# Kernel tuning notes

Hardware: AMD Instinct MI355X
Metric: run time of the kernel (lower is better)

Reference implementation:

```python
import jax, jax.numpy as jnp
import numpy as np
import math

NUM_ITER = 5
FEAT_STRIDE = 16
GAUSS_SIGMA = 1.0
HINGE_THRESHOLD = -999.0
MIN_FILTER_REG = 1e-3
ALPHA_EPS = 0.0


def apply_filter(feat, weights):
    # feat: (ni, ns, C, H, W); weights: (ns, C, fH, fW) -> scores (ni, ns, oH, oW)
    ni, ns, C, H, W = feat.shape
    fH, fW = weights.shape[-2], weights.shape[-1]
    x = feat.reshape(ni, ns * C, H, W)
    out = jax.lax.conv_general_dilated(
        x, weights, window_strides=(1, 1),
        padding=((fH // 2, fH // 2), (fW // 2, fW // 2)),
        dimension_numbers=('NCHW', 'OIHW', 'NCHW'),
        feature_group_count=ns)
    return out  # (ni, ns, oH, oW); oH = H + (fH+1)%2


def get_label(center, out_sz, sigma):
    # center: (ni, ns, 2) in (row, col) order
    k0 = jnp.arange(out_sz[0], dtype=jnp.float32)[None, None, :, None]
    k1 = jnp.arange(out_sz[1], dtype=jnp.float32)[None, None, None, :]
    g0 = jnp.exp(-0.5 / (sigma * sigma) * (k0 - center[..., 0][..., None, None]) ** 2)
    g1 = jnp.exp(-0.5 / (sigma * sigma) * (k1 - center[..., 1][..., None, None]) ** 2)
    return g0 * g1  # (ni, ns, oH, oW)


def _forward(weights, feat, bb, log_step_length, filter_reg):
    ni, ns = feat.shape[0], feat.shape[1]
    fH, fW = weights.shape[-2], weights.shape[-1]
    out_sz = (feat.shape[-2] + (fH + 1) % 2, feat.shape[-1] + (fW + 1) % 2)
    step = jnp.exp(log_step_length)[0]
    reg = jnp.maximum(filter_reg * filter_reg, MIN_FILTER_REG ** 2)[0]
    dmap_offset = jnp.array([fH % 2, fW % 2], jnp.float32) / 2.0
    # (x, y) -> (row, col), feature-grid coordinates
    center = ((bb[..., :2] + bb[..., 2:] / 2.0) / FEAT_STRIDE)[..., ::-1] - dmap_offset
    label = get_label(center, out_sz, GAUSS_SIGMA)
    mask = (label > HINGE_THRESHOLD).astype(feat.dtype)
    label = label * mask
    sw = math.sqrt(1.0 / ni)

    losses = []
    for _ in range(NUM_ITER):
        scores = apply_filter(feat, weights)
        scores_act = mask * scores + (1.0 - mask) * jax.nn.relu(scores)
        score_mask = mask + (1.0 - mask) * (jax.lax.stop_gradient(scores) > 0).astype(scores.dtype)
        residuals = sw * (scores_act - label)
        losses.append((jnp.sum(residuals ** 2) + reg * jnp.sum(weights ** 2)) / ns)
        residuals_mapped = score_mask * (sw * residuals)
        # feat-transpose = adjoint of apply_filter w.r.t. the filter weights
        _, vjp_fn = jax.vjp(lambda w: apply_filter(feat, w), weights)
        data_grad = vjp_fn(residuals_mapped)[0]
        weights_grad = data_grad + reg * weights
        scores_grad = apply_filter(feat, weights_grad)
        scores_grad = sw * (score_mask * scores_grad)
        alpha_num = jnp.sum(weights_grad ** 2, axis=(1, 2, 3))  # (ns,)
        alpha_den = jnp.maximum(
            jnp.sum(scores_grad.reshape(ni, ns, -1) ** 2, axis=(0, 2))
            + (reg + ALPHA_EPS) * alpha_num, 1e-8)
        alpha = alpha_num / alpha_den
        weights = weights - step * alpha[:, None, None, None] * weights_grad

    scores = apply_filter(feat, weights)
    scores = mask * scores + (1.0 - mask) * jax.nn.relu(scores)
    losses.append((jnp.sum((sw * (scores - label)) ** 2) + reg * jnp.sum(weights ** 2)) / ns)
    return weights, jnp.stack(losses)


def setup_inputs() -> dict:
    key = jax.random.key(0)
    k1, k2, k3, k4 = jax.random.split(key, 4)
    ni, ns, C, H, W, fH, fW = 3, 32, 512, 22, 22, 4, 4
    weights = 0.01 * jax.random.normal(k1, (ns, C, fH, fW), jnp.float32)
    feat = jax.random.normal(k2, (ni, ns, C, H, W), jnp.float32)
    # boxes (x, y, w, h) in image coords (image size = 22*16 = 352)
    xy = jax.random.uniform(k3, (ni, ns, 2), jnp.float32, 50.0, 250.0)
    wh = jax.random.uniform(k4, (ni, ns, 2), jnp.float32, 32.0, 96.0)
    bb = jnp.concatenate([xy, wh], axis=-1)
    log_step_length = jnp.zeros((1,), jnp.float32)  # log(1.0)
    filter_reg = 0.01 * jnp.ones((1,), jnp.float32)
    return {"weights": weights, "feat": feat, "bb": bb,
            "log_step_length": log_step_length, "filter_reg": filter_reg}


def reference(weights, feat, bb, log_step_length, filter_reg):
    return _forward(weights, feat, bb, log_step_length, filter_reg)
```

## Files before the change

### kernel.cpp

```cpp
#include <hip/hip_runtime.h>
#include <hip/hip_fp16.h>

#define NI 3
#define NS 32
#define CHN 512
#define OH 23
#define P2 529
#define NP 50784
#define UV 484
#define WSZ 262144
#define KTOT 1536
#define NKB 48
#define RSP 1544

typedef unsigned int uint32;
typedef unsigned short u16;
typedef _Float16 h2 __attribute__((ext_vector_type(2)));
typedef _Float16 f16x8 __attribute__((ext_vector_type(8)));
typedef float f32x4 __attribute__((ext_vector_type(4)));

#define OFF_FEATT 0UL
#define OFF_LABEL 47579136UL
#define OFF_S0    47782272UL
#define OFF_S1    47985408UL
#define OFF_SGRAW 48188544UL
#define OFF_WG    48391680UL
#define OFF_WGF16 49440256UL
#define OFF_W0F16 49964544UL
#define OFF_PART  50488832UL
#define OFF_FEATC 50521600UL
#define OFF_S0B   100853248UL
#define OFF_SGB   101056384UL

#define P_DEN   0
#define P_NUM   4320
#define P_LOSS  5600
#define P_WSQ0  5760
#define P_WSQA  5792
#define P_WSQ5  6816
#define P_L5    7840

__device__ __forceinline__ float waveSum(float v) {
#pragma unroll
  for (int o = 32; o > 0; o >>= 1) v += __shfl_xor(v, o, 64);
  return v;
}

__global__ __launch_bounds__(256) void k_setup(const float* __restrict__ feat,
                                               const float* __restrict__ w0,
                                               const float* __restrict__ bb,
                                               u16* __restrict__ featT,
                                               u16* __restrict__ w0f16,
                                               float* __restrict__ wmaster,
                                               float* __restrict__ label,
                                               float* __restrict__ part) {
  __shared__ uint32 lds32[64 * 121];
  __shared__ float sred[4];
  int b = blockIdx.x, tid = threadIdx.x;
  if (b < 1536) {
    int snT = b >> 4, r4 = b & 15;
    int cb = r4 >> 1, uvh = r4 & 1;
    int s = snT / 3, n = snT % 3;
    const float* fsrc =
        feat + ((size_t)n * NS + s) * CHN * UV + (size_t)(cb * 64) * UV + uvh * 242;
#pragma unroll
    for (int it = 0; it < 31; ++it) {
      int idx = it * 256 + tid;
      if (idx < 7744) {
        int r = (unsigned)idx / 121u;
        int j = idx - r * 121;
        float2 v = *(const float2*)(fsrc + (size_t)r * UV + 2 * j);
        lds32[idx] = (uint32)__half_as_ushort(__float2half(v.x)) |
                     ((uint32)__half_as_ushort(__float2half(v.y)) << 16);
      }
    }
    __syncthreads();
    uint32* dstT = (uint32*)featT +
                   ((size_t)(snT * 4 + (cb >> 1)) * UV + uvh * 242) * 64 + (cb & 1) * 32;
#pragma unroll
    for (int it = 0; it < 16; ++it) {
      int o = it * 256 + tid;
      if (o < 3872) {
        int uv = o >> 4, kp = o & 15;
        int j = uv >> 1, sh = (uv & 1) * 16;
        uint32 a0 = lds32[(4 * kp + 0) * 121 + j];
        uint32 a1 = lds32[(4 * kp + 1) * 121 + j];
        uint32 a2 = lds32[(4 * kp + 2) * 121 + j];
        uint32 a3 = lds32[(4 * kp + 3) * 121 + j];
        uint2 val;
        val.x = ((a0 >> sh) & 0xffffu) | (((a1 >> sh) & 0xffffu) << 16);
        val.y = ((a2 >> sh) & 0xffffu) | (((a3 >> sh) & 0xffffu) << 16);
        *(uint2*)(dstT + (size_t)uv * 64 + 2 * kp) = val;
      }
    }
  } else if (b < 1568) {
    int s = b - 1536;
    for (int i = tid; i < 8192; i += 256) {
      int tap = i >> 9, c = i & 511;
      w0f16[(size_t)s * 8192 + i] =
          __half_as_ushort(__float2half(w0[(size_t)s * 8192 + c * 16 + tap]));
    }
    float sq = 0.f;
    for (int i = tid; i < 8192; i += 256) {
      float v = w0[(size_t)s * 8192 + i];
      wmaster[(size_t)s * 8192 + i] = v;
      sq += v * v;
    }
    sq = waveSum(sq);
    if ((tid & 63) == 0) sred[tid >> 6] = sq;
    __syncthreads();
    if (tid == 0) part[P_WSQ0 + s] = sred[0] + sred[1] + sred[2] + sred[3];
  } else {
    int p = (b - 1568) * 256 + tid;
    if (p < NP) {
      int nsid = p / P2, rem = p % P2;
      int i = rem / OH, j = rem % OH;
      const float* bp = bb + (size_t)nsid * 4;
      float cr = (bp[1] + 0.5f * bp[3]) * 0.0625f;
      float cc = (bp[0] + 0.5f * bp[2]) * 0.0625f;
      float dy = (float)i - cr, dx = (float)j - cc;
      label[p] = __expf(-0.5f * (dy * dy + dx * dx));
    }
  }
}

__global__ __launch_bounds__(1024) void k_conv_fwd(const u16* __restrict__ featT,
                                                   const u16* __restrict__ wf16,
                                                   float* __restrict__ outA,
                                                   float* __restrict__ outB) {
  __shared__ uint32 w_lds[16 * 132];
  __shared__ float G[496 * 17];
  int tid = threadIdx.x;
  int bidx = blockIdx.x;
  int snT = bidx >> 1, ch = bidx & 1;
  int s = snT / 3, n = snT - s * 3;
  const uint32* wsrc = (const uint32*)(wf16 + (size_t)s * 8192) + ch * 128;
  for (int i = tid; i < 2048; i += 1024) {
    int tap = i >> 7, p = i & 127;
    w_lds[tap * 132 + p] = wsrc[(size_t)tap * 256 + p];
  }
  __syncthreads();
  int wave = tid >> 6, lane = tid & 63;
  int q = lane >> 4, m16 = lane & 15;
  int t0 = wave, t1 = wave + 16;
  bool has2 = (t1 < 31);
  f32x4 acc0 = {0.f, 0.f, 0.f, 0.f}, acc1 = {0.f, 0.f, 0.f, 0.f};
  size_t base = (size_t)snT * 4 * UV * 128;
  int r0i = t0 * 16 + m16;
  int r1i = has2 ? t1 * 16 + m16 : 483;
  if (r1i > 483) r1i = 483;
  size_t row0 = (size_t)r0i * 128;
  size_t row1 = (size_t)r1i * 128;
#pragma unroll
  for (int ks = 0; ks < 8; ++ks) {
    int cb = ch * 2 + (ks >> 2), cin = (ks & 3) * 32;
    size_t cbase = base + (size_t)cb * UV * 128 + cin + q * 8;
    f16x8 a0 = *(const f16x8*)(featT + cbase + row0);
    uint4 bw = *(const uint4*)&w_lds[m16 * 132 + ks * 16 + q * 4];
    f16x8 bf = __builtin_bit_cast(f16x8, bw);
    acc0 = __builtin_amdgcn_mfma_f32_16x16x32_f16(a0, bf, acc0, 0, 0, 0);
    if (has2) {
      f16x8 a1 = *(const f16x8*)(featT + cbase + row1);
      acc1 = __builtin_amdgcn_mfma_f32_16x16x32_f16(a1, bf, acc1, 0, 0, 0);
    }
  }
#pragma unroll
  for (int r = 0; r < 4; ++r) G[(t0 * 16 + q * 4 + r) * 17 + m16] = acc0[r];
  if (has2) {
#pragma unroll
    for (int r = 0; r < 4; ++r) G[(t1 * 16 + q * 4 + r) * 17 + m16] = acc1[r];
  }
  __syncthreads();
  if (tid < P2) {
    int y = tid / 23, x = tid - y * 23;
    float val = 0.f;
#pragma unroll
    for (int ky = 0; ky < 4; ++ky) {
      int u = y + ky - 2;
      if ((unsigned)u < 22u) {
#pragma unroll
        for (int kx = 0; kx < 4; ++kx) {
          int v = x + kx - 2;
          if ((unsigned)v < 22u) val += G[(u * 22 + v) * 17 + ky * 4 + kx];
        }
      }
    }
    float* dst = ch ? outB : outA;
    dst[(size_t)(n * NS + s) * P2 + tid] = val;
  }
}

__global__ __launch_bounds__(1024) void k_adjoint(
    int t, const float* __restrict__ feat, u16* __restrict__ featC,
    const float* __restrict__ label, const float* __restrict__ s0a,
    const float* __restrict__ s0b, const float* __restrict__ scores_old,
    float* __restrict__ scores_new, const float* __restrict__ sga,
    const float* __restrict__ sgb, float* __restrict__ wg, u16* __restrict__ wgf16,
    float* __restrict__ wmaster, float* __restrict__ part, const float* __restrict__ lsl,
    const float* __restrict__ fr) {
  __shared__ float r_lds[3 * P2];
  __shared__ __align__(16) u16 rs[16 * RSP];
  __shared__ __align__(16) float kred[3 * 4 * 64 * 4];
  __shared__ float lred[16], nred[16], wred[16], dend[16];
  int tid = threadIdx.x;
  int s = blockIdx.x >> 3, chunk = blockIdx.x & 7;
  int c0 = chunk * 64;
  float step = __expf(lsl[0]);
  float frv = fr[0];
  float reg = fmaxf(frv * frv, 1e-6f);

  float alpha_p = 0.f;
  if (t >= 1) {
    const float* np_ = part + P_NUM + (size_t)((t - 1) * NS + s) * 8;
    float nu = 0.f;
#pragma unroll
    for (int i = 0; i < 8; ++i) nu += np_[i];
    float dp = 0.f;
    for (int pl = tid; pl < 1587; pl += 1024) {
      int nn = (unsigned)pl / (unsigned)P2;
      int rem = pl - nn * P2;
      size_t gp = (size_t)(nn * NS + s) * P2 + rem;
      float g = sga[gp] + sgb[gp];
      dp += g * g;
    }
    dp = waveSum(dp);
    if ((tid & 63) == 0) dend[tid >> 6] = dp;
    __syncthreads();
    float de = 0.f;
#pragma unroll
    for (int i = 0; i < 16; ++i) de += dend[i];
    alpha_p = nu / fmaxf(de * (1.0f / 3.0f) + reg * nu, 1e-8f);
  }

  float lsum = 0.f;
  for (int pl = tid; pl < 1587; pl += 1024) {
    int nn = (unsigned)pl / (unsigned)P2;
    int rem = pl - nn * P2;
    size_t gp = (size_t)(nn * NS + s) * P2 + rem;
    float S = (t <= 1) ? (s0a[gp] + s0b[gp]) : scores_old[gp];
    if (t >= 1) S -= step * alpha_p * (sga[gp] + sgb[gp]);
    float d = S - label[gp];
    r_lds[nn * P2 + rem] = d * (1.0f / 3.0f);
    if (chunk == 0) {
      if (t >= 1) scores_new[gp] = S;
      lsum += d * d;
    }
  }
  lsum = waveSum(lsum);
  if ((tid & 63) == 0) lred[tid >> 6] = lsum;
  __syncthreads();
  if (chunk == 0 && tid == 0) {
    float L = 0.f;
#pragma unroll
    for (int i = 0; i < 16; ++i) L += lred[i];
    part[P_LOSS + t * NS + s] = L * (1.0f / 3.0f);
  }

  for (int idx = tid; idx < 16 * RSP; idx += 1024) {
    int tap = (unsigned)idx / (unsigned)RSP;
    int k = idx - tap * RSP;
    float val = 0.f;
    if (k < KTOT) {
      int n = k >> 9, uv = k & 511;
      if (uv < UV) {
        int u = (unsigned)uv / 22u;
        int v = uv - u * 22;
        int ky = tap >> 2, kx = tap & 3;
        int y = u + 2 - ky, x = v + 2 - kx;
        if ((unsigned)y < 23u && (unsigned)x < 23u) val = r_lds[n * P2 + y * OH + x];
      }
    }
    rs[idx] = __half_as_ushort(__float2half(val));
  }
  __syncthreads();

  int wave = tid >> 6, lane = tid & 63;
  int q = lane >> 4, m16 = lane & 15;
  int tile = wave & 3, kq = wave >> 2;
  int c = c0 + tile * 16 + m16;
  const u16* brow = rs + m16 * RSP + kq * 384 + q * 8;
  f32x4 acc = {0.f, 0.f, 0.f, 0.f};
  if (t == 0) {
#pragma unroll
    for (int ks = 0; ks < 12; ++ks) {
      int kb = kq * 12 + ks;
      int k0 = kb * 32 + q * 8;
      int nn = k0 >> 9, uv0 = k0 & 511;
      float v[8];
#pragma unroll
      for (int i = 0; i < 8; ++i) v[i] = 0.f;
      if (uv0 < UV) {
        const float* fsrc = feat + ((size_t)(nn * NS + s) * CHN + c) * UV + uv0;
        if (uv0 + 8 <= UV) {
          float4 p0 = *(const float4*)fsrc;
          float4 p1 = *(const float4*)(fsrc + 4);
          v[0] = p0.x; v[1] = p0.y; v[2] = p0.z; v[3] = p0.w;
          v[4] = p1.x; v[5] = p1.y; v[6] = p1.z; v[7] = p1.w;
        } else {
#pragma unroll
          for (int i = 0; i < 4; ++i) v[i] = fsrc[i];
        }
      }
      union { u16 h[8]; f16x8 f; uint4 u; } av;
#pragma unroll
      for (int i = 0; i < 8; ++i) av.h[i] = __half_as_ushort(__float2half(v[i]));
      *(uint4*)(featC + (((size_t)(s * NKB + kb) * CHN + c) * 32 + q * 8)) = av.u;
      f16x8 bf = *(const f16x8*)(brow + ks * 32);
      acc = __builtin_amdgcn_mfma_f32_16x16x32_f16(av.f, bf, acc, 0, 0, 0);
    }
  } else {
    const u16* arow = featC + ((size_t)(s * NKB + kq * 12) * CHN + c) * 32 + q * 8;
#pragma unroll
    for (int ks = 0; ks < 12; ++ks) {
      f16x8 a = *(const f16x8*)(arow + (size_t)ks * (CHN * 32));
      f16x8 bf = *(const f16x8*)(brow + ks * 32);
      acc = __builtin_amdgcn_mfma_f32_16x16x32_f16(a, bf, acc, 0, 0, 0);
    }
  }
  if (kq) *(f32x4*)&kred[(((kq - 1) * 4 + tile) * 64 + lane) * 4] = acc;
  __syncthreads();

  float num_part = 0.f, wsq_part = 0.f;
  if (kq == 0) {
#pragma unroll
    for (int kk = 0; kk < 3; ++kk)
      acc += *(const f32x4*)&kred[((kk * 4 + tile) * 64 + lane) * 4];
    int tap = m16;
    int ccb = c0 + tile * 16 + q * 4;
    union { u16 h[4]; uint2 v2; } pk;
#pragma unroll
    for (int r = 0; r < 4; ++r) {
      int cc = ccb + r;
      size_t widx = (size_t)s * 8192 + (size_t)cc * 16 + tap;
      float wold = wmaster[widx];
      float wnew = wold;
      if (t >= 1) {
        wnew = wold - step * alpha_p * wg[widx];
        wmaster[widx] = wnew;
      }
      float wgn = acc[r] + reg * wnew;
      wg[widx] = wgn;
      pk.h[r] = __half_as_ushort(__float2half(wgn));
      wsq_part += wnew * wnew;
      num_part += wgn * wgn;
    }
    *(uint2*)&wgf16[(size_t)s * 8192 + (size_t)tap * 512 + ccb] = pk.v2;
  }
  num_part = waveSum(num_part);
  wsq_part = waveSum(wsq_part);
  if (lane == 0) {
    nred[wave] = num_part;
    wred[wave] = wsq_part;
  }
  __syncthreads();
  if (tid == 0) {
    float nsum = 0.f, wsum = 0.f;
#pragma unroll
    for (int i = 0; i < 16; ++i) {
      nsum += nred[i];
      wsum += wred[i];
    }
    part[P_NUM + (size_t)(t * NS + s) * 8 + chunk] = nsum;
    if (t >= 1) part[P_WSQA + (size_t)((t - 1) * NS + s) * 8 + chunk] = wsum;
  }
}

__global__ __launch_bounds__(1024) void k_den(const float* __restrict__ sga,
                                              const float* __restrict__ sgb,
                                              float* __restrict__ part) {
  __shared__ float dend[16];
  int s = blockIdx.x, tid = threadIdx.x;
  float dp = 0.f;
  for (int pl = tid; pl < 1587; pl += 1024) {
    int nn = (unsigned)pl / (unsigned)P2;
    int rem = pl - nn * P2;
    size_t gp = (size_t)(nn * NS + s) * P2 + rem;
    float g = sga[gp] + sgb[gp];
    dp += g * g;
  }
  dp = waveSum(dp);
  if ((tid & 63) == 0) dend[tid >> 6] = dp;
  __syncthreads();
  if (tid == 0) {
    float de = 0.f;
#pragma unroll
    for (int i = 0; i < 16; ++i) de += dend[i];
    part[P_DEN + s] = de * (1.0f / 3.0f);
  }
}

__device__ __forceinline__ float alphaFinal(const float* __restrict__ part, int s,
                                            float reg) {
  const float* np_ = part + P_NUM + (size_t)(4 * NS + s) * 8;
  float nu = 0.f;
#pragma unroll
  for (int i = 0; i < 8; ++i) nu += np_[i];
  float de = part[P_DEN + s];
  return nu / fmaxf(de + reg * nu, 1e-8f);
}

__global__ void k_final(float* __restrict__ wmaster, const float* __restrict__ wg,
                        const float* __restrict__ scores4, const float* __restrict__ sga,
                        const float* __restrict__ sgb, const float* __restrict__ label,
                        float* __restrict__ part, const float* __restrict__ lsl,
                        const float* __restrict__ fr) {
  __shared__ float alpha_s[32];
  __shared__ float red4[4];
  int b = blockIdx.x, tid = threadIdx.x;
  float step = __expf(lsl[0]);
  float frv = fr[0];
  float reg = fmaxf(frv * frv, 1e-6f);
  if (tid < 32) alpha_s[tid] = alphaFinal(part, tid, reg);
  __syncthreads();
  if (b < 1024) {
    int idx = b * 256 + tid;
    int s = idx >> 13;
    float w5 = wmaster[idx] - step * alpha_s[s] * wg[idx];
    wmaster[idx] = w5;
    float sq = waveSum(w5 * w5);
    if ((tid & 63) == 0) red4[tid >> 6] = sq;
    __syncthreads();
    if (tid == 0) part[P_WSQ5 + b] = red4[0] + red4[1] + red4[2] + red4[3];
  } else {
    int p = (b - 1024) * 256 + tid;
    float contrib = 0.f;
    if (p < NP) {
      int nsid = p / P2;
      int s = nsid & 31;
      float s5 = scores4[p] - step * alpha_s[s] * (sga[p] + sgb[p]);
      float d = s5 - label[p];
      contrib = d * d;
    }
    contrib = waveSum(contrib);
    if ((tid & 63) == 0) red4[tid >> 6] = contrib;
    __syncthreads();
    if (tid == 0)
      part[P_L5 + (b - 1024)] = (red4[0] + red4[1] + red4[2] + red4[3]) * (1.0f / 3.0f);
  }
}

__global__ void k_losses(float* __restrict__ out_losses, const float* __restrict__ part,
                         const float* __restrict__ fr) {
  __shared__ float red[8];
  int tid = threadIdx.x;
  float frv = fr[0];
  float reg = fmaxf(frv * frv, 1e-6f);
  float v5 = 0.f;
  for (int i = tid; i < 1024; i += 256) v5 += part[P_WSQ5 + i];
  v5 = waveSum(v5);
  if ((tid & 63) == 0) red[tid >> 6] = v5;
  __syncthreads();
  float wsq5 = red[0] + red[1] + red[2] + red[3];
  float l5 = 0.f;
  for (int i = tid; i < 199; i += 256) l5 += part[P_L5 + i];
  l5 = waveSum(l5);
  if ((tid & 63) == 0) red[4 + (tid >> 6)] = l5;
  __syncthreads();
  float loss5 = red[4] + red[5] + red[6] + red[7];
  if (tid < 5) {
    int t = tid;
    float ls = 0.f;
    for (int i = 0; i < 32; ++i) ls += part[P_LOSS + t * NS + i];
    float ws_ = 0.f;
    if (t == 0) {
      for (int i = 0; i < 32; ++i) ws_ += part[P_WSQ0 + i];
    } else {
      for (int i = 0; i < 256; ++i) ws_ += part[P_WSQA + (t - 1) * 256 + i];
    }
    out_losses[t] = (ls + reg * ws_) * (1.0f / 32.0f);
  }
  if (tid == 5) out_losses[5] = (loss5 + reg * wsq5) * (1.0f / 32.0f);
}

extern "C" void kernel_launch(void* const* d_in, const int* in_sizes, int n_in,
                              void* d_out, int out_size, void* d_ws, size_t ws_size,
                              hipStream_t stream) {
  const float* w0 = (const float*)d_in[0];
  const float* feat = (const float*)d_in[1];
  const float* bb = (const float*)d_in[2];
  const float* lsl = (const float*)d_in[3];
  const float* fr = (const float*)d_in[4];
  float* out = (float*)d_out;
  char* ws = (char*)d_ws;
  u16* featT = (u16*)(ws + OFF_FEATT);
  float* label = (float*)(ws + OFF_LABEL);
  float* s0 = (float*)(ws + OFF_S0);
  float* s0b = (float*)(ws + OFF_S0B);
  float* s1 = (float*)(ws + OFF_S1);
  float* sga = (float*)(ws + OFF_SGRAW);
  float* sgb = (float*)(ws + OFF_SGB);
  float* wg = (float*)(ws + OFF_WG);
  u16* wgf16 = (u16*)(ws + OFF_WGF16);
  u16* w0f16 = (u16*)(ws + OFF_W0F16);
  float* part = (float*)(ws + OFF_PART);
  u16* featC = (u16*)(ws + OFF_FEATC);

  k_setup<<<1767, 256, 0, stream>>>(feat, w0, bb, featT, w0f16, out, label, part);
  k_conv_fwd<<<192, 1024, 0, stream>>>(featT, w0f16, s0, s0b);
  for (int t = 0; t < 5; ++t) {
    const float* so = (t <= 1) ? s0 : ((t & 1) ? s0 : s1);
    float* sn = (t & 1) ? s1 : s0;
    k_adjoint<<<256, 1024, 0, stream>>>(t, feat, featC, label, s0, s0b, so, sn, sga, sgb,
                                        wg, wgf16, out, part, lsl, fr);
    k_conv_fwd<<<192, 1024, 0, stream>>>(featT, wgf16, sga, sgb);
  }
  k_den<<<32, 1024, 0, stream>>>(sga, sgb, part);
  k_final<<<1223, 256, 0, stream>>>(out, wg, s0, sga, sgb, label, part, lsl, fr);
  k_losses<<<1, 256, 0, stream>>>(out + WSZ, part, fr);
}
```

Before: 356.1 us.

## Fuse k_den and k_losses into k_final with per-block alpha and ticket reduction

Removes the separate k_den and k_losses launches. Each k_final block now recomputes its spectrum's step-length denominator locally, and the last block to finish, found with an atomic ticket counter, does the final loss reduction. k_adjoint also caches the summed gradient scores in LDS so they are not reloaded from global memory. In exchange, 1223 blocks now each re-read 1587 gradient values, the atomic ticket adds a completion step, and k_adjoint uses more LDS.

```diff
diff --git a/kernel.cpp b/kernel.cpp
--- a/kernel.cpp
+++ b/kernel.cpp
@@ -32,13 +32,13 @@
 #define OFF_S0B   100853248UL
 #define OFF_SGB   101056384UL
 
-#define P_DEN   0
 #define P_NUM   4320
 #define P_LOSS  5600
 #define P_WSQ0  5760
 #define P_WSQA  5792
 #define P_WSQ5  6816
 #define P_L5    7840
+#define P_TICKET 8064
 
 __device__ __forceinline__ float waveSum(float v) {
 #pragma unroll
@@ -95,6 +95,7 @@
     }
   } else if (b < 1568) {
     int s = b - 1536;
+    if (b == 1536 && tid == 0) ((uint32*)part)[P_TICKET] = 0;
     for (int i = tid; i < 8192; i += 256) {
       int tap = i >> 9, c = i & 511;
       w0f16[(size_t)s * 8192 + i] =
@@ -199,6 +200,7 @@
     float* __restrict__ wmaster, float* __restrict__ part, const float* __restrict__ lsl,
     const float* __restrict__ fr) {
   __shared__ float r_lds[3 * P2];
+  __shared__ float g_lds[1587];
   __shared__ __align__(16) u16 rs[16 * RSP];
   __shared__ __align__(16) float kred[3 * 4 * 64 * 4];
   __shared__ float lred[16], nred[16], wred[16], dend[16];
@@ -221,6 +223,7 @@
       int rem = pl - nn * P2;
       size_t gp = (size_t)(nn * NS + s) * P2 + rem;
       float g = sga[gp] + sgb[gp];
+      g_lds[pl] = g;
       dp += g * g;
     }
     dp = waveSum(dp);
@@ -238,7 +241,7 @@
     int rem = pl - nn * P2;
     size_t gp = (size_t)(nn * NS + s) * P2 + rem;
     float S = (t <= 1) ? (s0a[gp] + s0b[gp]) : scores_old[gp];
-    if (t >= 1) S -= step * alpha_p * (sga[gp] + sgb[gp]);
+    if (t >= 1) S -= step * alpha_p * g_lds[pl];
     float d = S - label[gp];
     r_lds[nn * P2 + rem] = d * (1.0f / 3.0f);
     if (chunk == 0) {
@@ -365,13 +368,12 @@
   }
 }
 
-__global__ __launch_bounds__(1024) void k_den(const float* __restrict__ sga,
-                                              const float* __restrict__ sgb,
-                                              float* __restrict__ part) {
-  __shared__ float dend[16];
-  int s = blockIdx.x, tid = threadIdx.x;
+__device__ __forceinline__ float blockAlpha(int s, const float* __restrict__ sga,
+                                            const float* __restrict__ sgb,
+                                            const float* __restrict__ part, float reg,
+                                            int tid, float* ared) {
   float dp = 0.f;
-  for (int pl = tid; pl < 1587; pl += 1024) {
+  for (int pl = tid; pl < 1587; pl += 256) {
     int nn = (unsigned)pl / (unsigned)P2;
     int rem = pl - nn * P2;
     size_t gp = (size_t)(nn * NS + s) * P2 + rem;
@@ -379,97 +381,98 @@
     dp += g * g;
   }
   dp = waveSum(dp);
-  if ((tid & 63) == 0) dend[tid >> 6] = dp;
-  __syncthreads();
-  if (tid == 0) {
-    float de = 0.f;
-#pragma unroll
-    for (int i = 0; i < 16; ++i) de += dend[i];
-    part[P_DEN + s] = de * (1.0f / 3.0f);
-  }
-}
-
-__device__ __forceinline__ float alphaFinal(const float* __restrict__ part, int s,
-                                            float reg) {
+  __syncthreads();
+  if ((tid & 63) == 0) ared[tid >> 6] = dp;
+  __syncthreads();
+  float de = (ared[0] + ared[1] + ared[2] + ared[3]) * (1.0f / 3.0f);
   const float* np_ = part + P_NUM + (size_t)(4 * NS + s) * 8;
   float nu = 0.f;
 #pragma unroll
   for (int i = 0; i < 8; ++i) nu += np_[i];
-  float de = part[P_DEN + s];
   return nu / fmaxf(de + reg * nu, 1e-8f);
 }
 
-__global__ void k_final(float* __restrict__ wmaster, const float* __restrict__ wg,
-                        const float* __restrict__ scores4, const float* __restrict__ sga,
-                        const float* __restrict__ sgb, const float* __restrict__ label,
-                        float* __restrict__ part, const float* __restrict__ lsl,
-                        const float* __restrict__ fr) {
-  __shared__ float alpha_s[32];
+__global__ __launch_bounds__(256) void k_final(
+    float* __restrict__ wmaster, const float* __restrict__ wg,
+    const float* __restrict__ scores4, const float* __restrict__ sga,
+    const float* __restrict__ sgb, const float* __restrict__ label,
+    float* __restrict__ part, const float* __restrict__ lsl,
+    const float* __restrict__ fr, float* __restrict__ out_losses) {
+  __shared__ float aredS[4];
   __shared__ float red4[4];
+  __shared__ uint32 tkt_s;
   int b = blockIdx.x, tid = threadIdx.x;
   float step = __expf(lsl[0]);
   float frv = fr[0];
   float reg = fmaxf(frv * frv, 1e-6f);
-  if (tid < 32) alpha_s[tid] = alphaFinal(part, tid, reg);
-  __syncthreads();
   if (b < 1024) {
+    int s = b >> 5;
+    float alpha = blockAlpha(s, sga, sgb, part, reg, tid, aredS);
     int idx = b * 256 + tid;
-    int s = idx >> 13;
-    float w5 = wmaster[idx] - step * alpha_s[s] * wg[idx];
+    float w5 = wmaster[idx] - step * alpha * wg[idx];
     wmaster[idx] = w5;
     float sq = waveSum(w5 * w5);
+    __syncthreads();
     if ((tid & 63) == 0) red4[tid >> 6] = sq;
     __syncthreads();
     if (tid == 0) part[P_WSQ5 + b] = red4[0] + red4[1] + red4[2] + red4[3];
   } else {
-    int p = (b - 1024) * 256 + tid;
+    int p0 = (b - 1024) * 256;
+    int nsid0 = (unsigned)p0 / (unsigned)P2;
+    int plast = p0 + 255;
+    if (plast > NP - 1) plast = NP - 1;
+    int nsid1 = (unsigned)plast / (unsigned)P2;
+    float alphaA = blockAlpha(nsid0 & 31, sga, sgb, part, reg, tid, aredS);
+    float alphaB = alphaA;
+    if (nsid1 != nsid0) alphaB = blockAlpha(nsid1 & 31, sga, sgb, part, reg, tid, aredS);
+    int p = p0 + tid;
     float contrib = 0.f;
     if (p < NP) {
-      int nsid = p / P2;
-      int s = nsid & 31;
-      float s5 = scores4[p] - step * alpha_s[s] * (sga[p] + sgb[p]);
+      int nsid = (unsigned)p / (unsigned)P2;
+      float alpha = (nsid == nsid0) ? alphaA : alphaB;
+      float s5 = scores4[p] - step * alpha * (sga[p] + sgb[p]);
       float d = s5 - label[p];
       contrib = d * d;
     }
     contrib = waveSum(contrib);
+    __syncthreads();
     if ((tid & 63) == 0) red4[tid >> 6] = contrib;
     __syncthreads();
     if (tid == 0)
       part[P_L5 + (b - 1024)] = (red4[0] + red4[1] + red4[2] + red4[3]) * (1.0f / 3.0f);
   }
-}
-
-__global__ void k_losses(float* __restrict__ out_losses, const float* __restrict__ part,
-                         const float* __restrict__ fr) {
-  __shared__ float red[8];
-  int tid = threadIdx.x;
-  float frv = fr[0];
-  float reg = fmaxf(frv * frv, 1e-6f);
-  float v5 = 0.f;
-  for (int i = tid; i < 1024; i += 256) v5 += part[P_WSQ5 + i];
-  v5 = waveSum(v5);
-  if ((tid & 63) == 0) red[tid >> 6] = v5;
-  __syncthreads();
-  float wsq5 = red[0] + red[1] + red[2] + red[3];
-  float l5 = 0.f;
-  for (int i = tid; i < 199; i += 256) l5 += part[P_L5 + i];
-  l5 = waveSum(l5);
-  if ((tid & 63) == 0) red[4 + (tid >> 6)] = l5;
-  __syncthreads();
-  float loss5 = red[4] + red[5] + red[6] + red[7];
-  if (tid < 5) {
-    int t = tid;
-    float ls = 0.f;
-    for (int i = 0; i < 32; ++i) ls += part[P_LOSS + t * NS + i];
-    float ws_ = 0.f;
-    if (t == 0) {
-      for (int i = 0; i < 32; ++i) ws_ += part[P_WSQ0 + i];
-    } else {
-      for (int i = 0; i < 256; ++i) ws_ += part[P_WSQA + (t - 1) * 256 + i];
-    }
-    out_losses[t] = (ls + reg * ws_) * (1.0f / 32.0f);
-  }
-  if (tid == 5) out_losses[5] = (loss5 + reg * wsq5) * (1.0f / 32.0f);
+  __threadfence();
+  __syncthreads();
+  if (tid == 0) tkt_s = atomicAdd((uint32*)&part[P_TICKET], 1u);
+  __syncthreads();
+  if (tkt_s == 1222) {
+    __threadfence();
+    float v5 = 0.f;
+    for (int i = tid; i < 1024; i += 256) v5 += part[P_WSQ5 + i];
+    v5 = waveSum(v5);
+    if ((tid & 63) == 0) red4[tid >> 6] = v5;
+    __syncthreads();
+    float wsq5 = red4[0] + red4[1] + red4[2] + red4[3];
+    float l5 = 0.f;
+    for (int i = tid; i < 199; i += 256) l5 += part[P_L5 + i];
+    l5 = waveSum(l5);
+    if ((tid & 63) == 0) aredS[tid >> 6] = l5;
+    __syncthreads();
+    float loss5 = aredS[0] + aredS[1] + aredS[2] + aredS[3];
+    if (tid < 5) {
+      int t = tid;
+      float ls = 0.f;
+      for (int i = 0; i < 32; ++i) ls += part[P_LOSS + t * NS + i];
+      float ws_ = 0.f;
+      if (t == 0) {
+        for (int i = 0; i < 32; ++i) ws_ += part[P_WSQ0 + i];
+      } else {
+        for (int i = 0; i < 256; ++i) ws_ += part[P_WSQA + (t - 1) * 256 + i];
+      }
+      out_losses[t] = (ls + reg * ws_) * (1.0f / 32.0f);
+    }
+    if (tid == 5) out_losses[5] = (loss5 + reg * wsq5) * (1.0f / 32.0f);
+  }
 }
 
 extern "C" void kernel_launch(void* const* d_in, const int* in_sizes, int n_in,
@@ -504,7 +507,6 @@
                                         wg, wgf16, out, part, lsl, fr);
     k_conv_fwd<<<192, 1024, 0, stream>>>(featT, wgf16, sga, sgb);
   }
-  k_den<<<32, 1024, 0, stream>>>(sga, sgb, part);
-  k_final<<<1223, 256, 0, stream>>>(out, wg, s0, sga, sgb, label, part, lsl, fr);
-  k_losses<<<1, 256, 0, stream>>>(out + WSZ, part, fr);
-}
+  k_final<<<1223, 256, 0, stream>>>(out, wg, s0, sga, sgb, label, part, lsl, fr,
+                                    out + WSZ);
+}
```

Result: slower. 435.2 us (+22.2%).
